# Performance work log

Measured on AMD Instinct MI355X. Metric: run time of the kernel, lower is better.

The kernel has to match this reference:

```python
import jax, jax.numpy as jnp
from jax import lax
import numpy as np

PAD_IDX = 4
KERNEL_SIZES = (2, 3, 4, 5)
N_FILTERS = 32
D_EMB = 8
D_OUT = 64
VOCAB = 5
B, L = 4096, 512
LN_EPS = 1e-5


def setup_inputs() -> dict:
    key = jax.random.key(0)
    ks = jax.random.split(key, 32)
    inp = {}
    inp['x_idx'] = jax.random.randint(ks[0], (B, L), 0, VOCAB, dtype=jnp.int64 if jax.config.jax_enable_x64 else jnp.int32)
    emb = jax.random.normal(ks[1], (VOCAB, D_EMB), dtype=jnp.float32) * 0.1
    inp['emb'] = emb.at[PAD_IDX].set(0.0)  # padding_idx row zero
    for i, kz in enumerate(KERNEL_SIZES):
        inp[f'conv_w{i}'] = jax.random.normal(ks[2 + 2 * i], (N_FILTERS, D_EMB, kz), dtype=jnp.float32) * (1.0 / np.sqrt(D_EMB * kz))
        inp[f'conv_b{i}'] = jnp.zeros((N_FILTERS,), jnp.float32)
        inp[f'att_w{i}'] = jax.random.normal(ks[3 + 2 * i], (N_FILTERS,), dtype=jnp.float32) * (1.0 / np.sqrt(N_FILTERS))
        inp[f'att_b{i}'] = jnp.zeros((1,), jnp.float32)
    inp['proj_w'] = jax.random.normal(ks[20], (D_OUT, N_FILTERS * len(KERNEL_SIZES)), dtype=jnp.float32) * (1.0 / np.sqrt(N_FILTERS * len(KERNEL_SIZES)))
    inp['proj_b'] = jnp.zeros((D_OUT,), jnp.float32)
    inp['gamma'] = jnp.ones((D_OUT,), jnp.float32)
    inp['beta'] = jnp.zeros((D_OUT,), jnp.float32)
    return inp


def _branch(X, W, b, aw, ab):
    # X: [B, C_in, L]; W: [C_out, C_in, ks]
    h = lax.conv_general_dilated(X, W, (1,), 'VALID',
                                 dimension_numbers=('NCH', 'OIH', 'NCH'))
    h = jax.nn.gelu(h + b[None, :, None], approximate=False)     # [B, F, L']
    scores = jnp.einsum('bfl,f->bl', h, aw) + ab[0]              # linear attn score
    w = jax.nn.softmax(scores, axis=1)                           # over positions
    return jnp.einsum('bfl,bl->bf', h, w)                        # weighted pool -> [B, F]


def reference(x_idx, emb, conv_w0, conv_b0, conv_w1, conv_b1, conv_w2, conv_b2,
              conv_w3, conv_b3, att_w0, att_b0, att_w1, att_b1, att_w2, att_b2,
              att_w3, att_b3, proj_w, proj_b, gamma, beta):
    emb = emb.at[PAD_IDX].set(0.0)
    X = emb[x_idx].transpose(0, 2, 1)  # [B, d_emb, L]
    feats = [
        _branch(X, conv_w0, conv_b0, att_w0, att_b0),
        _branch(X, conv_w1, conv_b1, att_w1, att_b1),
        _branch(X, conv_w2, conv_b2, att_w2, att_b2),
        _branch(X, conv_w3, conv_b3, att_w3, att_b3),
    ]
    z = jnp.concatenate(feats, axis=1)                 # [B, 4*F]
    z = z @ proj_w.T + proj_b                          # [B, D_OUT]
    z = jax.nn.gelu(z, approximate=False)
    mu = jnp.mean(z, axis=-1, keepdims=True)
    var = jnp.var(z, axis=-1, keepdims=True)
    return (z - mu) / jnp.sqrt(var + LN_EPS) * gamma + beta
```

## Files before the change

kernel.cpp:

```cpp
#include <hip/hip_runtime.h>
#include <math.h>

typedef _Float16 half_t;
typedef _Float16 half8 __attribute__((ext_vector_type(8)));
typedef unsigned short ushort_t;

#define BATCH 4096
#define SEQL  512
#define NF    32
#define DEMB  8
#define DOUT  64

#define NWIN_TOTAL 3900
#define HWIN_OFF   4096
#define ETAB_OFF   67000
#define TOFF       70000
#define EHE_OFF    131072
#define MSHIFT     8.0f

__device__ __forceinline__ float gelu_exact(float x) {
    return 0.5f * x * (1.0f + erff(x * 0.70710678118654752f));
}

__global__ __launch_bounds__(256) void precompute_taps(
    const float* __restrict__ emb,
    const float* __restrict__ cw0, const float* __restrict__ cw1,
    const float* __restrict__ cw2, const float* __restrict__ cw3,
    float* __restrict__ ws)
{
    const int gid = blockIdx.x * blockDim.x + threadIdx.x;
    if (gid >= 14 * 5 * NF) return;
    const int f = gid & 31;
    const int r = gid >> 5;
    const int tapg = r / 5;
    const int d    = r % 5;

    int ks, t; const float* cw;
    if (tapg < 2)      { ks = 2; cw = cw0; t = tapg; }
    else if (tapg < 5) { ks = 3; cw = cw1; t = tapg - 2; }
    else if (tapg < 9) { ks = 4; cw = cw2; t = tapg - 5; }
    else               { ks = 5; cw = cw3; t = tapg - 9; }

    const float* e = emb + d * DEMB;
    float s = 0.0f;
#pragma unroll
    for (int c = 0; c < DEMB; ++c)
        s += e[c] * cw[(f * DEMB + c) * ks + t];
    ws[TOFF + r * NF + f] = s;
}

__global__ __launch_bounds__(256) void precompute_windows(
    const float* __restrict__ cb0, const float* __restrict__ aw0, const float* __restrict__ ab0,
    const float* __restrict__ cb1, const float* __restrict__ aw1, const float* __restrict__ ab1,
    const float* __restrict__ cb2, const float* __restrict__ aw2, const float* __restrict__ ab2,
    const float* __restrict__ cb3, const float* __restrict__ aw3, const float* __restrict__ ab3,
    float* __restrict__ ws)
{
    const int gid = blockIdx.x * blockDim.x + threadIdx.x;
    if (gid >= NWIN_TOTAL * NF) return;
    const int wgid = gid >> 5;
    const int f    = gid & 31;

    int w, ks, cum;
    const float *cb, *aw, *ab;
    if (wgid < 25)       { w = wgid;       ks = 2; cum = 0; cb = cb0; aw = aw0; ab = ab0; }
    else if (wgid < 150) { w = wgid - 25;  ks = 3; cum = 2; cb = cb1; aw = aw1; ab = ab1; }
    else if (wgid < 775) { w = wgid - 150; ks = 4; cum = 5; cb = cb2; aw = aw2; ab = ab2; }
    else                 { w = wgid - 775; ks = 5; cum = 9; cb = cb3; aw = aw3; ab = ab3; }

    float h = cb[f];
    int ww = w;
    for (int t = ks - 1; t >= 0; --t) {
        int d = ww % 5; ww /= 5;
        h += ws[TOFF + ((cum + t) * 5 + d) * NF + f];
    }
    float g = gelu_exact(h);
    ((half_t*)(ws + HWIN_OFF))[wgid * NF + f] = (half_t)g;

    float s = g * aw[f];
#pragma unroll
    for (int off = 16; off; off >>= 1) s += __shfl_xor(s, off, 32);
    if (f == 0)
        ((half_t*)(ws + ETAB_OFF))[wgid] = (half_t)__expf(s + ab[0] - MSHIFT);
}

__global__ __launch_bounds__(256) void build_combined(float* __restrict__ ws)
{
    const int gid = blockIdx.x * blockDim.x + threadIdx.x;
    if (gid >= 3125 * 16) return;
    const int w5  = gid >> 4;
    const int seg = gid & 15;
    const int c   = seg >> 2;
    const int q   = seg & 3;

    int wc, swb;
    if (c == 0)      { wc = w5 / 125; swb = 0;   }
    else if (c == 1) { wc = w5 / 25;  swb = 25;  }
    else if (c == 2) { wc = w5 / 5;   swb = 150; }
    else             { wc = w5;       swb = 775; }
    const int gw = swb + wc;

    const float E = (float)((const half_t*)(ws + ETAB_OFF))[gw];
    const half_t* hp = (const half_t*)(ws + HWIN_OFF) + gw * NF + q * 8;
    half_t o[8];
#pragma unroll
    for (int j = 0; j < 8; ++j) o[j] = (half_t)(E * (float)hp[j]);
    *(float4*)((char*)(ws + EHE_OFF) + w5 * 256 + seg * 16) = *(const float4*)o;
}

__global__ __launch_bounds__(256) void fused_main(
    const int*   __restrict__ xidx,
    const float* __restrict__ ws,
    const float* __restrict__ projw, const float* __restrict__ projb,
    const float* __restrict__ gamma, const float* __restrict__ beta,
    float* __restrict__ out)
{
    __shared__ int      xs[SEQL + 8];
    __shared__ ushort_t pwid[SEQL];
    __shared__ float    partial[4][16][8];
    __shared__ float    redD[4][4];
    __shared__ float    feat[4 * NF];

    const int b   = blockIdx.x;
    const int tid = threadIdx.x;

#pragma unroll
    for (int i = tid; i < SEQL / 4; i += 256)
        ((int4*)xs)[i] = ((const int4*)(xidx + b * SEQL))[i];
    if (tid < 8) xs[SEQL + tid] = 0;
    __syncthreads();

    const int wave = tid >> 6;
    const int lane = tid & 63;
    const half_t* Etab = (const half_t*)(ws + ETAB_OFF);

    float den0 = 0.f, den1 = 0.f, den2 = 0.f, den3 = 0.f;
#pragma unroll
    for (int it = 0; it < 2; ++it) {
        const int l = wave * 128 + it * 64 + lane;
        const int w2 = xs[l] * 5 + xs[l + 1];
        const int w3 = w2 * 5 + xs[l + 2];
        const int w4 = w3 * 5 + xs[l + 3];
        const int w5 = w4 * 5 + xs[l + 4];
        pwid[l] = (ushort_t)w5;
        if (l < 511) den0 += (float)Etab[w2];
        if (l < 510) den1 += (float)Etab[25 + w3];
        if (l < 509) den2 += (float)Etab[150 + w4];
        if (l < 508) den3 += (float)Etab[775 + w5];
    }
#pragma unroll
    for (int off = 32; off; off >>= 1) {
        den0 += __shfl_xor(den0, off);
        den1 += __shfl_xor(den1, off);
        den2 += __shfl_xor(den2, off);
        den3 += __shfl_xor(den3, off);
    }
    if (lane == 0) {
        redD[wave][0] = den0; redD[wave][1] = den1;
        redD[wave][2] = den2; redD[wave][3] = den3;
    }
    __syncthreads();

    const int seg = lane & 15;
    const int o   = lane >> 4;
    const int c   = seg >> 2;
    const int Lpc = 511 - c;
    const char* base = (const char*)(ws + EHE_OFF) + seg * 16;

    float a[8];
#pragma unroll
    for (int j = 0; j < 8; ++j) a[j] = 0.0f;

#pragma unroll 8
    for (int it = 0; it < 32; ++it) {
        const int pos = wave * 128 + it * 4 + o;
        const int w5 = pwid[pos];
        if (pos < Lpc) {
            const float4 rv = *(const float4*)(base + w5 * 256);
            const half8 hv = *(const half8*)&rv;
#pragma unroll
            for (int j = 0; j < 8; ++j) a[j] += (float)hv[j];
        }
    }

#pragma unroll
    for (int j = 0; j < 8; ++j) {
        a[j] += __shfl_xor(a[j], 16);
        a[j] += __shfl_xor(a[j], 32);
    }
    if (lane < 16) {
#pragma unroll
        for (int j = 0; j < 8; ++j) partial[wave][lane][j] = a[j];
    }
    __syncthreads();

    if (tid < 128) {
        const int sg = tid >> 3, j = tid & 7, cc = tid >> 5;
        const float d = redD[0][cc] + redD[1][cc] + redD[2][cc] + redD[3][cc];
        feat[tid] = (partial[0][sg][j] + partial[1][sg][j]
                   + partial[2][sg][j] + partial[3][sg][j]) / d;
    }
    __syncthreads();

    if (tid < DOUT) {
        float z = projb[tid];
        const float4* pwr = (const float4*)(projw + tid * (4 * NF));
#pragma unroll
        for (int q = 0; q < 32; ++q) {
            float4 wq = pwr[q];
            const float* fj = feat + q * 4;
            z += wq.x * fj[0] + wq.y * fj[1] + wq.z * fj[2] + wq.w * fj[3];
        }
        z = gelu_exact(z);

        float s1 = z, s2 = z * z;
#pragma unroll
        for (int off = 32; off; off >>= 1) {
            s1 += __shfl_xor(s1, off);
            s2 += __shfl_xor(s2, off);
        }
        const float mu  = s1 * (1.0f / 64.0f);
        const float var = s2 * (1.0f / 64.0f) - mu * mu;
        const float rr  = rsqrtf(var + 1e-5f);
        out[b * DOUT + tid] = (z - mu) * rr * gamma[tid] + beta[tid];
    }
}

extern "C" void kernel_launch(void* const* d_in, const int* in_sizes, int n_in,
                              void* d_out, int out_size, void* d_ws, size_t ws_size,
                              hipStream_t stream) {
    const int*   xidx = (const int*)d_in[0];
    const float* emb  = (const float*)d_in[1];
    const float* cw[4]; const float* cb[4]; const float* aw[4]; const float* ab[4];
    for (int i = 0; i < 4; ++i) {
        cw[i] = (const float*)d_in[2 + 4 * i];
        cb[i] = (const float*)d_in[3 + 4 * i];
        aw[i] = (const float*)d_in[4 + 4 * i];
        ab[i] = (const float*)d_in[5 + 4 * i];
    }
    const float* projw = (const float*)d_in[18];
    const float* projb = (const float*)d_in[19];
    const float* gm    = (const float*)d_in[20];
    const float* bt    = (const float*)d_in[21];
    float* ws  = (float*)d_ws;
    float* out = (float*)d_out;

    hipLaunchKernelGGL(precompute_taps, dim3((14 * 5 * NF + 255) / 256), dim3(256), 0, stream,
                       emb, cw[0], cw[1], cw[2], cw[3], ws);

    hipLaunchKernelGGL(precompute_windows, dim3((NWIN_TOTAL * NF + 255) / 256), dim3(256), 0, stream,
                       cb[0], aw[0], ab[0],
                       cb[1], aw[1], ab[1],
                       cb[2], aw[2], ab[2],
                       cb[3], aw[3], ab[3],
                       ws);

    hipLaunchKernelGGL(build_combined, dim3((3125 * 16 + 255) / 256), dim3(256), 0, stream,
                       ws);

    hipLaunchKernelGGL(fused_main, dim3(BATCH), dim3(256), 0, stream,
                       xidx, ws, projw, projb, gm, bt, out);
}
```

Baseline: 146.4 us.

## Split gather tables: LDS-resident k=2/3 tables, halve global k=4/5 row size

Replaces the single 256-byte combined table indexed by 5-gram id with a 128-byte table covering only the k=4 and k=5 branches. The k=2 and k=3 weighted-hidden tables and all exp tables are staged into shared memory per block, and their gathers run from LDS. A max_score kernel now subtracts the actual maximum score in place of a fixed shift, which improves numerical safety. The aim is to halve global/L2 gather traffic in the main loop, at the cost of per-block LDS staging (~20KB), extra launches and a second accumulation pass.

Result: slower. 171.2 us (+16.9%).

```diff
diff --git a/kernel.cpp b/kernel.cpp
--- a/kernel.cpp
+++ b/kernel.cpp
@@ -2,8 +2,8 @@
 #include <math.h>
 
 typedef _Float16 half_t;
-typedef _Float16 half8 __attribute__((ext_vector_type(8)));
 typedef unsigned short ushort_t;
+typedef unsigned char u8;
 
 #define BATCH 4096
 #define SEQL  512
@@ -12,11 +12,18 @@
 #define DOUT  64
 
 #define NWIN_TOTAL 3900
+#define MAXS_OFF   3968
 #define HWIN_OFF   4096
-#define ETAB_OFF   67000
 #define TOFF       70000
-#define EHE_OFF    131072
-#define MSHIFT     8.0f
+#define B_EH45     524288
+#define B_EH2      1048576
+#define B_EH3      1050376
+#define B_E2       1059376
+#define B_E3       1059440
+#define B_E4       1059696
+#define B_E5       1060976
+
+union U8h { uint2 u; half_t h[4]; };
 
 __device__ __forceinline__ float gelu_exact(float x) {
     return 0.5f * x * (1.0f + erff(x * 0.70710678118654752f));
@@ -80,32 +87,71 @@
     float s = g * aw[f];
 #pragma unroll
     for (int off = 16; off; off >>= 1) s += __shfl_xor(s, off, 32);
-    if (f == 0)
-        ((half_t*)(ws + ETAB_OFF))[wgid] = (half_t)__expf(s + ab[0] - MSHIFT);
-}
-
-__global__ __launch_bounds__(256) void build_combined(float* __restrict__ ws)
+    if (f == 0) ws[wgid] = s + ab[0];
+}
+
+__global__ __launch_bounds__(256) void max_score(float* __restrict__ ws)
+{
+    __shared__ float red[4];
+    float m = -1e30f;
+    for (int i = threadIdx.x; i < NWIN_TOTAL; i += 256) m = fmaxf(m, ws[i]);
+#pragma unroll
+    for (int off = 32; off; off >>= 1) m = fmaxf(m, __shfl_xor(m, off));
+    if ((threadIdx.x & 63) == 0) red[threadIdx.x >> 6] = m;
+    __syncthreads();
+    if (threadIdx.x == 0)
+        ws[MAXS_OFF] = fmaxf(fmaxf(red[0], red[1]), fmaxf(red[2], red[3]));
+}
+
+__global__ __launch_bounds__(256) void build_eh45(float* __restrict__ ws)
 {
     const int gid = blockIdx.x * blockDim.x + threadIdx.x;
     if (gid >= 3125 * 16) return;
     const int w5  = gid >> 4;
     const int seg = gid & 15;
-    const int c   = seg >> 2;
-    const int q   = seg & 3;
-
-    int wc, swb;
-    if (c == 0)      { wc = w5 / 125; swb = 0;   }
-    else if (c == 1) { wc = w5 / 25;  swb = 25;  }
-    else if (c == 2) { wc = w5 / 5;   swb = 150; }
-    else             { wc = w5;       swb = 775; }
-    const int gw = swb + wc;
-
-    const float E = (float)((const half_t*)(ws + ETAB_OFF))[gw];
-    const half_t* hp = (const half_t*)(ws + HWIN_OFF) + gw * NF + q * 8;
-    half_t o[8];
-#pragma unroll
-    for (int j = 0; j < 8; ++j) o[j] = (half_t)(E * (float)hp[j]);
-    *(float4*)((char*)(ws + EHE_OFF) + w5 * 256 + seg * 16) = *(const float4*)o;
+    const int br  = seg >> 3;
+    const int q   = seg & 7;
+    const int gw  = br ? (775 + w5) : (150 + w5 / 5);
+
+    const float m = ws[MAXS_OFF];
+    const float E = __expf(ws[gw] - m);
+    const half_t* hp = (const half_t*)(ws + HWIN_OFF) + gw * NF + q * 4;
+    U8h v;
+#pragma unroll
+    for (int j = 0; j < 4; ++j) v.h[j] = (half_t)(E * (float)hp[j]);
+    *(uint2*)((char*)ws + B_EH45 + w5 * 128 + seg * 8) = v.u;
+}
+
+__global__ __launch_bounds__(256) void build_small(float* __restrict__ ws)
+{
+    const int gid = blockIdx.x * blockDim.x + threadIdx.x;
+    const float m = ws[MAXS_OFF];
+
+    if (gid < 4800) {
+        const int row = gid >> 5;
+        const int f   = gid & 31;
+        int gw; half_t* dst; half_t* edst;
+        if (row < 25) {
+            gw  = row;
+            dst = (half_t*)((char*)ws + B_EH2) + row * 36 + f;
+            edst= (half_t*)((char*)ws + B_E2) + row;
+        } else {
+            const int w3 = row - 25;
+            gw  = 25 + w3;
+            dst = (half_t*)((char*)ws + B_EH3) + w3 * 36 + f;
+            edst= (half_t*)((char*)ws + B_E3) + w3;
+        }
+        const float E = __expf(ws[gw] - m);
+        const float h = (float)((const half_t*)(ws + HWIN_OFF))[gw * NF + f];
+        *dst = (half_t)(E * h);
+        if (f == 0) *edst = (half_t)E;
+    } else if (gid < 5425) {
+        const int w4 = gid - 4800;
+        ((half_t*)((char*)ws + B_E4))[w4] = (half_t)__expf(ws[150 + w4] - m);
+    } else if (gid < 8550) {
+        const int w5 = gid - 5425;
+        ((half_t*)((char*)ws + B_E5))[w5] = (half_t)__expf(ws[775 + w5] - m);
+    }
 }
 
 __global__ __launch_bounds__(256) void fused_main(
@@ -116,8 +162,13 @@
     float* __restrict__ out)
 {
     __shared__ int      xs[SEQL + 8];
-    __shared__ ushort_t pwid[SEQL];
-    __shared__ float    partial[4][16][8];
+    __shared__ ushort_t w5id[SEQL];
+    __shared__ u8       w2id[SEQL], w3id[SEQL];
+    __shared__ half_t   eh2S[25 * 36];
+    __shared__ half_t   eh3S[125 * 36];
+    __shared__ half_t   e2S[32], e3S[128], e4S[640], e5S[3136];
+    __shared__ float    partial45[4][16][4];
+    __shared__ float    partial2[4][8][4], partial3[4][8][4];
     __shared__ float    redD[4][4];
     __shared__ float    feat[4 * NF];
 
@@ -128,77 +179,137 @@
     for (int i = tid; i < SEQL / 4; i += 256)
         ((int4*)xs)[i] = ((const int4*)(xidx + b * SEQL))[i];
     if (tid < 8) xs[SEQL + tid] = 0;
+    {
+        const unsigned* g;
+        g = (const unsigned*)((const char*)ws + B_EH2);
+        for (int i = tid; i < 450;  i += 256) ((unsigned*)eh2S)[i] = g[i];
+        g = (const unsigned*)((const char*)ws + B_EH3);
+        for (int i = tid; i < 2250; i += 256) ((unsigned*)eh3S)[i] = g[i];
+        g = (const unsigned*)((const char*)ws + B_E2);
+        if (tid < 16) ((unsigned*)e2S)[tid] = g[tid];
+        g = (const unsigned*)((const char*)ws + B_E3);
+        if (tid < 64) ((unsigned*)e3S)[tid] = g[tid];
+        g = (const unsigned*)((const char*)ws + B_E4);
+        for (int i = tid; i < 320;  i += 256) ((unsigned*)e4S)[i] = g[i];
+        g = (const unsigned*)((const char*)ws + B_E5);
+        for (int i = tid; i < 1568; i += 256) ((unsigned*)e5S)[i] = g[i];
+    }
     __syncthreads();
 
     const int wave = tid >> 6;
     const int lane = tid & 63;
-    const half_t* Etab = (const half_t*)(ws + ETAB_OFF);
-
-    float den0 = 0.f, den1 = 0.f, den2 = 0.f, den3 = 0.f;
-#pragma unroll
-    for (int it = 0; it < 2; ++it) {
-        const int l = wave * 128 + it * 64 + lane;
-        const int w2 = xs[l] * 5 + xs[l + 1];
-        const int w3 = w2 * 5 + xs[l + 2];
-        const int w4 = w3 * 5 + xs[l + 3];
-        const int w5 = w4 * 5 + xs[l + 4];
-        pwid[l] = (ushort_t)w5;
-        if (l < 511) den0 += (float)Etab[w2];
-        if (l < 510) den1 += (float)Etab[25 + w3];
-        if (l < 509) den2 += (float)Etab[150 + w4];
-        if (l < 508) den3 += (float)Etab[775 + w5];
-    }
-#pragma unroll
-    for (int off = 32; off; off >>= 1) {
-        den0 += __shfl_xor(den0, off);
-        den1 += __shfl_xor(den1, off);
-        den2 += __shfl_xor(den2, off);
-        den3 += __shfl_xor(den3, off);
-    }
-    if (lane == 0) {
-        redD[wave][0] = den0; redD[wave][1] = den1;
-        redD[wave][2] = den2; redD[wave][3] = den3;
-    }
-    __syncthreads();
-
-    const int seg = lane & 15;
-    const int o   = lane >> 4;
-    const int c   = seg >> 2;
-    const int Lpc = 511 - c;
-    const char* base = (const char*)(ws + EHE_OFF) + seg * 16;
-
-    float a[8];
-#pragma unroll
-    for (int j = 0; j < 8; ++j) a[j] = 0.0f;
-
+
+    {
+        float den2 = 0.f, den3 = 0.f, den4 = 0.f, den5 = 0.f;
+#pragma unroll
+        for (int it = 0; it < 2; ++it) {
+            const int l = wave * 128 + it * 64 + lane;
+            const int w2 = xs[l] * 5 + xs[l + 1];
+            const int w3 = w2 * 5 + xs[l + 2];
+            const int w4 = w3 * 5 + xs[l + 3];
+            const int w5 = w4 * 5 + xs[l + 4];
+            w5id[l] = (ushort_t)w5;
+            w2id[l] = (u8)w2;
+            w3id[l] = (u8)w3;
+            if (l < 511) den2 += (float)e2S[w2];
+            if (l < 510) den3 += (float)e3S[w3];
+            if (l < 509) den4 += (float)e4S[w4];
+            if (l < 508) den5 += (float)e5S[w5];
+        }
+#pragma unroll
+        for (int off = 32; off; off >>= 1) {
+            den2 += __shfl_xor(den2, off);
+            den3 += __shfl_xor(den3, off);
+            den4 += __shfl_xor(den4, off);
+            den5 += __shfl_xor(den5, off);
+        }
+        if (lane == 0) {
+            redD[wave][0] = den2; redD[wave][1] = den3;
+            redD[wave][2] = den4; redD[wave][3] = den5;
+        }
+    }
+    __syncthreads();
+
+    {
+        const int o4  = lane >> 4;
+        const int seg = lane & 15;
+        const char* baseA = (const char*)ws + B_EH45 + seg * 8;
+        const int limA = (seg < 8) ? 509 : 508;
+
+        float a[4] = {0.f, 0.f, 0.f, 0.f};
 #pragma unroll 8
-    for (int it = 0; it < 32; ++it) {
-        const int pos = wave * 128 + it * 4 + o;
-        const int w5 = pwid[pos];
-        if (pos < Lpc) {
-            const float4 rv = *(const float4*)(base + w5 * 256);
-            const half8 hv = *(const half8*)&rv;
-#pragma unroll
-            for (int j = 0; j < 8; ++j) a[j] += (float)hv[j];
-        }
-    }
-
-#pragma unroll
-    for (int j = 0; j < 8; ++j) {
-        a[j] += __shfl_xor(a[j], 16);
-        a[j] += __shfl_xor(a[j], 32);
-    }
-    if (lane < 16) {
-#pragma unroll
-        for (int j = 0; j < 8; ++j) partial[wave][lane][j] = a[j];
+        for (int it = 0; it < 32; ++it) {
+            const int pos = wave * 128 + it * 4 + o4;
+            const int w5 = w5id[pos];
+            if (pos < limA) {
+                U8h v; v.u = *(const uint2*)(baseA + w5 * 128);
+#pragma unroll
+                for (int j = 0; j < 4; ++j) a[j] += (float)v.h[j];
+            }
+        }
+#pragma unroll
+        for (int j = 0; j < 4; ++j) {
+            a[j] += __shfl_xor(a[j], 16);
+            a[j] += __shfl_xor(a[j], 32);
+        }
+        if (lane < 16) {
+#pragma unroll
+            for (int j = 0; j < 4; ++j) partial45[wave][seg][j] = a[j];
+        }
+    }
+
+    {
+        const int o8 = lane >> 3;
+        const int r8 = lane & 7;
+        float a2[4] = {0.f, 0.f, 0.f, 0.f};
+        float a3[4] = {0.f, 0.f, 0.f, 0.f};
+#pragma unroll 4
+        for (int it = 0; it < 16; ++it) {
+            const int pos = wave * 128 + it * 8 + o8;
+            const int w2 = w2id[pos];
+            const int w3 = w3id[pos];
+            if (pos < 511) {
+                U8h v; v.u = *(const uint2*)((const char*)eh2S + w2 * 72 + r8 * 8);
+#pragma unroll
+                for (int j = 0; j < 4; ++j) a2[j] += (float)v.h[j];
+            }
+            if (pos < 510) {
+                U8h v; v.u = *(const uint2*)((const char*)eh3S + w3 * 72 + r8 * 8);
+#pragma unroll
+                for (int j = 0; j < 4; ++j) a3[j] += (float)v.h[j];
+            }
+        }
+#pragma unroll
+        for (int j = 0; j < 4; ++j) {
+            a2[j] += __shfl_xor(a2[j], 8);  a3[j] += __shfl_xor(a3[j], 8);
+            a2[j] += __shfl_xor(a2[j], 16); a3[j] += __shfl_xor(a3[j], 16);
+            a2[j] += __shfl_xor(a2[j], 32); a3[j] += __shfl_xor(a3[j], 32);
+        }
+        if (lane < 8) {
+#pragma unroll
+            for (int j = 0; j < 4; ++j) {
+                partial2[wave][lane][j] = a2[j];
+                partial3[wave][lane][j] = a3[j];
+            }
+        }
     }
     __syncthreads();
 
     if (tid < 128) {
-        const int sg = tid >> 3, j = tid & 7, cc = tid >> 5;
-        const float d = redD[0][cc] + redD[1][cc] + redD[2][cc] + redD[3][cc];
-        feat[tid] = (partial[0][sg][j] + partial[1][sg][j]
-                   + partial[2][sg][j] + partial[3][sg][j]) / d;
+        const int c = tid >> 5;
+        const int f = tid & 31;
+        const int r = f >> 2, j = f & 3;
+        float num;
+        if (c == 0)      num = partial2[0][r][j] + partial2[1][r][j]
+                             + partial2[2][r][j] + partial2[3][r][j];
+        else if (c == 1) num = partial3[0][r][j] + partial3[1][r][j]
+                             + partial3[2][r][j] + partial3[3][r][j];
+        else if (c == 2) num = partial45[0][r][j] + partial45[1][r][j]
+                             + partial45[2][r][j] + partial45[3][r][j];
+        else             num = partial45[0][8 + r][j] + partial45[1][8 + r][j]
+                             + partial45[2][8 + r][j] + partial45[3][8 + r][j];
+        const float d = redD[0][c] + redD[1][c] + redD[2][c] + redD[3][c];
+        feat[tid] = num / d;
     }
     __syncthreads();
 
@@ -255,8 +366,11 @@
                        cb[3], aw[3], ab[3],
                        ws);
 
-    hipLaunchKernelGGL(build_combined, dim3((3125 * 16 + 255) / 256), dim3(256), 0, stream,
-                       ws);
+    hipLaunchKernelGGL(max_score, dim3(1), dim3(256), 0, stream, ws);
+
+    hipLaunchKernelGGL(build_eh45, dim3((3125 * 16 + 255) / 256), dim3(256), 0, stream, ws);
+
+    hipLaunchKernelGGL(build_small, dim3((8550 + 255) / 256), dim3(256), 0, stream, ws);
 
     hipLaunchKernelGGL(fused_main, dim3(BATCH), dim3(256), 0, stream,
                        xidx, ws, projw, projb, gm, bt, out);
```
